# Kernel tuning notes

Hardware: AMD Instinct MI355X
Metric: run time of the kernel (lower is better)

Reference implementation:

```python
import jax, jax.numpy as jnp
import numpy as np

HIDDEN = 1024
HEADS = 16
DEPTH = HIDDEN // HEADS  # 64
B, S = 1, 2048  # batch must be 1: E is built with shape (heads, B*S, depth) and the skew reshape assumes B*S == S


def setup_inputs() -> dict:
    key = jax.random.key(0)
    ks = jax.random.split(key, 6)
    std = 0.02
    x = jax.random.normal(ks[0], (B, S, HIDDEN), dtype=jnp.float32)
    c_attn_w = jax.random.normal(ks[1], (HIDDEN, 3 * HIDDEN), dtype=jnp.float32) * std
    c_attn_b = jnp.zeros((1, 3 * HIDDEN), dtype=jnp.float32)
    c_proj_w = jax.random.normal(ks[2], (HIDDEN, HIDDEN), dtype=jnp.float32) * std
    c_proj_b = jnp.zeros((1, HIDDEN), dtype=jnp.float32)
    # GlorotUniform for E of shape (heads, B*S, depth)
    limit = float(np.sqrt(6.0 / (B * S + DEPTH)))
    E = jax.random.uniform(ks[3], (HEADS, B * S, DEPTH), dtype=jnp.float32,
                           minval=-limit, maxval=limit)
    return {"x": x, "c_attn_w": c_attn_w, "c_attn_b": c_attn_b,
            "c_proj_w": c_proj_w, "c_proj_b": c_proj_b, "E": E}


def _split_heads(t):
    # [B,S,H] -> [B,heads,S,depth]
    b, s, h = t.shape
    return t.reshape(b, s, HEADS, h // HEADS).transpose(0, 2, 1, 3)


def _relative_attention(q, E):
    # Transformer-XL style skewing. q: [B,heads,S,depth], E: [heads,B*S,depth]
    b, h, s, d = q.shape
    q_ = q.transpose(1, 0, 2, 3).reshape(h, b * s, d)
    rel = jnp.einsum('hnd,hmd->hnm', q_, E)            # [h, B*S, B*S]
    rel = rel.reshape(h, b, s, s)
    rel = jnp.pad(rel, ((0, 0), (0, 0), (0, 0), (1, 0)))  # pad left on last dim
    rel = rel.reshape(h, b, s + 1, s)[:, :, 1:]            # skew
    return rel.transpose(1, 0, 2, 3)                       # [B,heads,S,S]


def reference(x, c_attn_w, c_attn_b, c_proj_w, c_proj_b, E):
    b, s, hidden = x.shape
    qkv = x @ c_attn_w + c_attn_b                      # [B,S,3H]
    q, k, v = jnp.split(qkv, 3, axis=2)
    q, k, v = _split_heads(q), _split_heads(k), _split_heads(v)  # [B,h,S,d]

    w = jnp.einsum('bhqd,bhkd->bhqk', q, k)            # raw scores
    w = w + _relative_attention(q, E)
    w = w * jax.lax.rsqrt(jnp.asarray(DEPTH, w.dtype))  # scale applied after rel bias

    # causal mask: 1 in lower triangle (i >= j - ns + nd, nd == ns == S)
    i = jnp.arange(s)[:, None]
    j = jnp.arange(s)[None, :]
    bmask = (i >= j).astype(w.dtype)[None, None]        # [1,1,S,S]
    w = w * bmask - 10000.0 * (1.0 - bmask)

    a = jax.nn.softmax(w, axis=-1)                      # dropout is identity at inference
    ctx = jnp.einsum('bhqk,bhkd->bhqd', a, v)
    ctx = ctx.transpose(0, 2, 1, 3).reshape(b, s, hidden)  # merge heads
    out = ctx @ c_proj_w + c_proj_b
    return out
```

## Files before the change

### kernel.cpp

```cpp
#include <hip/hip_runtime.h>
#include <math.h>

#define SEQ  2048
#define NH   16
#define DEP  64
#define HID  1024

typedef __attribute__((ext_vector_type(8))) short s16x8;
typedef __attribute__((ext_vector_type(4))) float f32x4;

#define MFMA16(a, b, c) __builtin_amdgcn_mfma_f32_16x16x32_bf16(a, b, c, 0, 0, 0)
#define GLDS16(g, l)                                                           \
  __builtin_amdgcn_global_load_lds(                                            \
      (const __attribute__((address_space(1))) void*)(g),                      \
      (__attribute__((address_space(3))) void*)(l), 16, 0, 0)

__device__ __forceinline__ ushort f2b(float f) {
  union { float f; unsigned u; } x; x.f = f;
  unsigned r = (x.u + 0x7fff + ((x.u >> 16) & 1)) >> 16;
  return (ushort)r;
}
__device__ __forceinline__ float b2f(ushort u) {
  union { unsigned u; float f; } x; x.u = ((unsigned)u) << 16;
  return x.f;
}

__global__ __launch_bounds__(256) void prep(
    const float* __restrict__ x, ushort* __restrict__ xb,
    const float* __restrict__ E, ushort* __restrict__ Eb,
    const float* __restrict__ Wa, ushort* __restrict__ Wat,
    const float* __restrict__ Wp, ushort* __restrict__ Wpt) {
  const int bid = blockIdx.x, t = threadIdx.x;
  if (bid < 1024) {
    __shared__ float Ls[64 * 68];
    const float* in; ushort* out; int C, tile;
    if (bid < 768) { in = Wa; out = Wat; C = 3072; tile = bid; }
    else           { in = Wp; out = Wpt; C = 1024; tile = bid - 768; }
    const int ntx = C / 64;
    const int n0 = (tile % ntx) * 64, k0 = (tile / ntx) * 64;
    const int r = t >> 4, c4 = t & 15;
    #pragma unroll
    for (int p = 0; p < 4; p++) {
      float4 v = *(const float4*)&in[(size_t)(k0 + r + 16 * p) * C + n0 + c4 * 4];
      *(float4*)&Ls[(r + 16 * p) * 68 + c4 * 4] = v;
    }
    __syncthreads();
    #pragma unroll
    for (int p = 0; p < 4; p++) {
      int rw = r + 16 * p;
      ushort4 o;
      o.x = f2b(Ls[(c4 * 4 + 0) * 68 + rw]);
      o.y = f2b(Ls[(c4 * 4 + 1) * 68 + rw]);
      o.z = f2b(Ls[(c4 * 4 + 2) * 68 + rw]);
      o.w = f2b(Ls[(c4 * 4 + 3) * 68 + rw]);
      *(ushort4*)&out[(size_t)(n0 + rw) * 1024 + k0 + c4 * 4] = o;
    }
  } else {
    const int id = bid - 1024;
    #pragma unroll
    for (int rep = 0; rep < 4; rep++) {
      int i = id * 256 + t + rep * 262144;
      const float* src; ushort* dst; int k;
      if (i < 524288) { src = x; dst = xb; k = i; }
      else            { src = E; dst = Eb; k = i - 524288; }
      float4 v = *(const float4*)&src[(size_t)k * 4];
      ushort4 o = {f2b(v.x), f2b(v.y), f2b(v.z), f2b(v.w)};
      *(ushort4*)&dst[(size_t)k * 4] = o;
    }
  }
}

__global__ __launch_bounds__(256, 3) void gemm_qkv(
    const ushort* __restrict__ A, const ushort* __restrict__ Bt,
    const float* __restrict__ bias, int N, int K,
    ushort* __restrict__ qd, ushort* __restrict__ kd, ushort* __restrict__ vt) {
  __shared__ ushort As[2][64 * 64];
  __shared__ ushort Bs[2][128 * 64];
  const int t = threadIdx.x, l = t & 63, w = t >> 6;
  const int lr = l & 15, quad = l >> 4;
  const int row8 = l >> 3;
  const int chunk = (l & 7) ^ ((l >> 3) & 7);
  const int m0 = blockIdx.y * 64, n0 = blockIdx.x * 128;
  const int wr = (w >> 1) * 32, wc = (w & 1) * 64;
  f32x4 acc[2][4] = {};
  const ushort* gA = A + (size_t)m0 * K + chunk * 8;
  const ushort* gB = Bt + (size_t)n0 * K + chunk * 8;

  auto issue = [&](int buf, int k0) {
    #pragma unroll
    for (int g = 0; g < 2; g++) {
      int r = 16 * w + 8 * g + row8;
      GLDS16(gA + (size_t)r * K + k0, &As[buf][(16 * w + 8 * g) * 64]);
    }
    #pragma unroll
    for (int g = 0; g < 4; g++) {
      int r = 32 * w + 8 * g + row8;
      GLDS16(gB + (size_t)r * K + k0, &Bs[buf][(32 * w + 8 * g) * 64]);
    }
  };

  issue(0, 0);
  const int nsteps = K / 64;
  for (int s = 0; s < nsteps; s++) {
    __syncthreads();
    if (s + 1 < nsteps) issue((s + 1) & 1, (s + 1) * 64);
    const char* as_ = (const char*)As[s & 1];
    const char* bs_ = (const char*)Bs[s & 1];
    s16x8 af[2][2], bf[4][2];
    #pragma unroll
    for (int i = 0; i < 2; i++)
      #pragma unroll
      for (int hh = 0; hh < 2; hh++)
        af[i][hh] = *(const s16x8*)(as_ + (wr + 16 * i + lr) * 128 +
                                    (((4 * hh + quad) ^ (lr & 7)) * 16));
    #pragma unroll
    for (int j = 0; j < 4; j++)
      #pragma unroll
      for (int hh = 0; hh < 2; hh++)
        bf[j][hh] = *(const s16x8*)(bs_ + (wc + 16 * j + lr) * 128 +
                                    (((4 * hh + quad) ^ (lr & 7)) * 16));
    #pragma unroll
    for (int i = 0; i < 2; i++)
      #pragma unroll
      for (int j = 0; j < 4; j++) {
        acc[i][j] = MFMA16(af[i][0], bf[j][0], acc[i][j]);
        acc[i][j] = MFMA16(af[i][1], bf[j][1], acc[i][j]);
      }
  }

  #pragma unroll
  for (int i = 0; i < 2; i++) {
    #pragma unroll
    for (int j = 0; j < 4; j++) {
      const int colg = n0 + wc + 16 * j + lr;
      const float bb = bias[colg];
      const int rowg0 = m0 + wr + 16 * i + 4 * quad;
      const int part = colg >> 10, hh = (colg >> 6) & 15, d = colg & 63;
      if (part == 2) {
        ushort4 ov;
        ov.x = f2b(acc[i][j][0] + bb);
        ov.y = f2b(acc[i][j][1] + bb);
        ov.z = f2b(acc[i][j][2] + bb);
        ov.w = f2b(acc[i][j][3] + bb);
        *(ushort4*)&vt[((size_t)hh * 64 + d) * SEQ + rowg0] = ov;
      } else {
        ushort* dst = part == 0 ? qd : kd;
        const float sc = part == 0 ? 0.125f : 1.0f;
        #pragma unroll
        for (int r = 0; r < 4; r++)
          dst[((size_t)hh * SEQ + rowg0 + r) * 64 + d] = f2b((acc[i][j][r] + bb) * sc);
      }
    }
  }
}

__global__ __launch_bounds__(256, 3) void gemm_proj(
    const ushort* __restrict__ A, const ushort* __restrict__ Bt,
    const float* __restrict__ bias, float* __restrict__ Cout,
    const ushort* __restrict__ po, const float* __restrict__ pl) {
  const int K = HID, N = HID;
  __shared__ ushort As[2][64 * 64];
  __shared__ ushort Bs[2][64 * 64];
  const int t = threadIdx.x, l = t & 63, w = t >> 6;
  const int lr = l & 15, quad = l >> 4;
  const int row8 = l >> 3;
  const int chunk = (l & 7) ^ ((l >> 3) & 7);
  const int m0 = blockIdx.y * 64, n0 = blockIdx.x * 64;
  const int wr = (w >> 1) * 32, wc = (w & 1) * 32;
  f32x4 acc[2][2] = {};
  const bool mergeA = (m0 >= 1024);
  const int pp = 31 - (m0 >> 6);
  const int mr = t >> 2, mseg = t & 3;
  int4 ra0, ra1, rb0, rb1; float rinv;
  const ushort* gA = A + (size_t)m0 * K + chunk * 8;
  const ushort* gB = Bt + (size_t)n0 * K + chunk * 8;

  auto issueA = [&](int buf, int k0) {
    #pragma unroll
    for (int g = 0; g < 2; g++) {
      int r = 16 * w + 8 * g;
      GLDS16(gA + (size_t)(r + row8) * K + k0, &As[buf][r * 64]);
    }
  };
  auto issueB = [&](int buf, int k0) {
    #pragma unroll
    for (int g = 0; g < 2; g++) {
      int r = 16 * w + 8 * g;
      GLDS16(gB + (size_t)(r + row8) * K + k0, &Bs[buf][r * 64]);
    }
  };
  auto stageA_load = [&](int k0) {
    const int hd = k0 >> 6;
    const ushort* o0 = po + ((size_t)(hd * 16 + pp) * 2) * 4096 + mr * 64 + mseg * 16;
    ra0 = *(const int4*)o0;
    ra1 = *(const int4*)(o0 + 8);
    rb0 = *(const int4*)(o0 + 4096);
    rb1 = *(const int4*)(o0 + 4096 + 8);
    const float* plb = pl + ((size_t)(hd * 16 + pp) * 2) * 64;
    rinv = 1.0f / (plb[mr] + plb[64 + mr]);
  };
  auto stageA_write = [&](int buf) {
    ushort* dst = &As[buf][mr * 64];
    ushort ov[8];
    const ushort* sa = (const ushort*)&ra0;
    const ushort* sb = (const ushort*)&rb0;
    #pragma unroll
    for (int k = 0; k < 8; k++) ov[k] = f2b((b2f(sa[k]) + b2f(sb[k])) * rinv);
    *(int4*)&dst[((2 * mseg) ^ (mr & 7)) * 8] = *(const int4*)ov;
    sa = (const ushort*)&ra1;
    sb = (const ushort*)&rb1;
    #pragma unroll
    for (int k = 0; k < 8; k++) ov[k] = f2b((b2f(sa[k]) + b2f(sb[k])) * rinv);
    *(int4*)&dst[((2 * mseg + 1) ^ (mr & 7)) * 8] = *(const int4*)ov;
  };

  if (mergeA) stageA_load(0); else issueA(0, 0);
  issueB(0, 0);
  if (mergeA) stageA_write(0);
  const int nsteps = K / 64;
  for (int s = 0; s < nsteps; s++) {
    __syncthreads();
    const bool pref = (s + 1 < nsteps);
    if (pref) {
      if (mergeA) stageA_load((s + 1) * 64);
      else issueA((s + 1) & 1, (s + 1) * 64);
      issueB((s + 1) & 1, (s + 1) * 64);
    }
    const char* as_ = (const char*)As[s & 1];
    const char* bs_ = (const char*)Bs[s & 1];
    s16x8 af[2][2], bf[2][2];
    #pragma unroll
    for (int i = 0; i < 2; i++)
      #pragma unroll
      for (int hh = 0; hh < 2; hh++)
        af[i][hh] = *(const s16x8*)(as_ + (wr + 16 * i + lr) * 128 +
                                    (((4 * hh + quad) ^ (lr & 7)) * 16));
    #pragma unroll
    for (int j = 0; j < 2; j++)
      #pragma unroll
      for (int hh = 0; hh < 2; hh++)
        bf[j][hh] = *(const s16x8*)(bs_ + (wc + 16 * j + lr) * 128 +
                                    (((4 * hh + quad) ^ (lr & 7)) * 16));
    #pragma unroll
    for (int i = 0; i < 2; i++)
      #pragma unroll
      for (int j = 0; j < 2; j++) {
        acc[i][j] = MFMA16(af[i][0], bf[j][0], acc[i][j]);
        acc[i][j] = MFMA16(af[i][1], bf[j][1], acc[i][j]);
      }
    if (pref && mergeA) stageA_write((s + 1) & 1);
  }

  #pragma unroll
  for (int i = 0; i < 2; i++)
    #pragma unroll
    for (int j = 0; j < 2; j++) {
      const int colg = n0 + wc + 16 * j + lr;
      const float bb = bias[colg];
      const int rowg0 = m0 + wr + 16 * i + 4 * quad;
      #pragma unroll
      for (int r = 0; r < 4; r++)
        Cout[(size_t)(rowg0 + r) * N + colg] = acc[i][j][r] + bb;
    }
}

__global__ __launch_bounds__(256, 2) void attn_mfma(
    const ushort* __restrict__ qw, const ushort* __restrict__ kw,
    const ushort* __restrict__ vT, const ushort* __restrict__ Ebf,
    ushort* __restrict__ ctx, ushort* __restrict__ pa_o,
    float* __restrict__ pa_l) {
  __shared__ ushort KT[2][64 * 64];
  __shared__ ushort VS[2][64 * 64];
  __shared__ ushort EB[4][64 * 64];
  __shared__ ushort PB[4][16 * 72];
  const int t = threadIdx.x, l = t & 63, w = t >> 6;
  const int lr = l & 15, quad = l >> 4;
  const int row8 = l >> 3;
  const int chunk = (l & 7) ^ ((l >> 3) & 7);
  const int h = blockIdx.y;
  const int p = blockIdx.x >> 1, half = blockIdx.x & 1;
  const int i0A = 64 * p, i0B = 64 * (31 - p);

  int ph_i0[2], ph_k0[2], ph_k1[2], nph, tot;
  bool ph_diag[2], ph_dir[2];
  if (half == 0) {
    ph_i0[0] = i0A; ph_k0[0] = 0; ph_k1[0] = p + 1;  ph_diag[0] = true;  ph_dir[0] = true;
    ph_i0[1] = i0B; ph_k0[1] = 0; ph_k1[1] = 16 - p; ph_diag[1] = false; ph_dir[1] = false;
    nph = 2; tot = 17;
  } else {
    ph_i0[0] = i0B; ph_k0[0] = 16 - p; ph_k1[0] = 32 - p; ph_diag[0] = true; ph_dir[0] = false;
    ph_i0[1] = 0; ph_k0[1] = 0; ph_k1[1] = 0; ph_diag[1] = false; ph_dir[1] = false;
    nph = 1; tot = 16;
  }

  const ushort* kwh = kw + (size_t)h * SEQ * 64;
  const ushort* vgh = vT + (size_t)h * 64 * SEQ;
  const ushort* egh = Ebf + (size_t)h * SEQ * 64;

  auto issue_kv = [&](int buf, int j0) {
    const ushort* kb = kwh + (size_t)j0 * 64 + chunk * 8;
    const ushort* vb = vgh + j0 + chunk * 8;
    #pragma unroll
    for (int g = 0; g < 2; g++) {
      int r = 16 * w + 8 * g + row8;
      GLDS16(kb + (size_t)r * 64, &KT[buf][(16 * w + 8 * g) * 64]);
      GLDS16(vb + (size_t)r * SEQ, &VS[buf][(16 * w + 8 * g) * 64]);
    }
  };
  auto issue_e = [&](int slot, int r0) {
    #pragma unroll
    for (int g = 0; g < 2; g++) {
      int r = r0 + 16 * w + 8 * g + row8;
      if (r > SEQ - 1) r = SEQ - 1;
      GLDS16(egh + (size_t)r * 64 + chunk * 8, &EB[slot][(16 * w + 8 * g) * 64]);
    }
  };

  int pi = 0, kt = ph_k0[0], ebs = 0;
  {
    const int m0 = 1984 - ph_i0[0] + kt * 64;
    issue_kv(0, kt * 64);
    issue_e(0, m0);
    issue_e(1, m0 + 64);
  }

  s16x8 aq0, aq1;
  {
    const ushort* qg = qw + ((size_t)h * SEQ + ph_i0[0] + 16 * w) * 64;
    aq0 = *(const s16x8*)(qg + lr * 64 + quad * 8);
    aq1 = *(const s16x8*)(qg + lr * 64 + 32 + quad * 8);
  }

  f32x4 o[4] = {};
  float li[4] = {0.f, 0.f, 0.f, 0.f};
  f32x4 rtc = {};

  for (int s = 0; s < tot; s++) {
    __syncthreads();

    const int i0 = ph_i0[pi];
    const bool first = (kt == ph_k0[pi]);
    const bool last = (kt == ph_k1[pi] - 1);
    const bool diag = ph_diag[pi] && last;

    int ebs_next = ebs;
    {
      int npi = pi, nkt = kt + 1;
      bool have = true, newph = false;
      if (nkt == ph_k1[pi]) {
        if (pi + 1 < nph) { npi = pi + 1; nkt = ph_k0[npi]; newph = true; }
        else have = false;
      }
      if (have) {
        issue_kv((s + 1) & 1, nkt * 64);
        const int m0n = 1984 - ph_i0[npi] + nkt * 64;
        if (newph) {
          issue_e((ebs + 2) & 3, m0n);
          issue_e((ebs + 3) & 3, m0n + 64);
          ebs_next = (ebs + 2) & 3;
        } else {
          issue_e((ebs + 2) & 3, m0n + 64);
          ebs_next = (ebs + 1) & 3;
        }
      }
    }

    const char* KTc = (const char*)KT[s & 1];
    const char* VSc = (const char*)VS[s & 1];

    auto eb_frag = [&](int row, s16x8& e0, s16x8& e1) {
      const char* e_ = (const char*)EB[(ebs + (row >> 6)) & 3];
      const int rb = (row & 63) * 128;
      e0 = *(const s16x8*)(e_ + rb + ((quad ^ (lr & 7)) * 16));
      e1 = *(const s16x8*)(e_ + rb + (((4 + quad) ^ (lr & 7)) * 16));
    };

    f32x4 s4[4];
    #pragma unroll
    for (int b = 0; b < 4; b++) {
      const int row = 16 * b + lr;
      s16x8 bk0 = *(const s16x8*)(KTc + row * 128 + ((quad ^ (lr & 7)) * 16));
      s16x8 bk1 = *(const s16x8*)(KTc + row * 128 + (((4 + quad) ^ (lr & 7)) * 16));
      f32x4 z = {};
      z = MFMA16(aq0, bk0, z);
      z = MFMA16(aq1, bk1, z);
      s4[b] = z;
    }

    {
      const int ebase = 48 - 16 * w;
      f32x4 rt[5];
      if (first) {
        s16x8 e0, e1;
        eb_frag(ebase + lr, e0, e1);
        f32x4 z = {};
        z = MFMA16(aq0, e0, z);
        z = MFMA16(aq1, e1, z);
        rt[0] = z;
      } else {
        rt[0] = rtc;
      }
      #pragma unroll
      for (int b = 1; b < 5; b++) {
        s16x8 e0, e1;
        eb_frag(ebase + 16 * b + lr, e0, e1);
        f32x4 z = {};
        z = MFMA16(aq0, e0, z);
        z = MFMA16(aq1, e1, z);
        rt[b] = z;
      }
      rtc = rt[4];
      #pragma unroll
      for (int r = 0; r < 4; r++) {
        const int ti = 4 * quad + r;
        const int u = lr - ti + 15;
        const int src = (u & 15) | (l & 48);
        const float sh0 = __shfl(rt[0][r], src);
        const float sh1 = __shfl(rt[1][r], src);
        const float sh2 = __shfl(rt[2][r], src);
        const float sh3 = __shfl(rt[3][r], src);
        const float sh4 = __shfl(rt[4][r], src);
        s4[0][r] += (u < 16) ? sh0 : sh1;
        s4[1][r] += (u < 16) ? sh1 : sh2;
        s4[2][r] += (u < 16) ? sh2 : sh3;
        s4[3][r] += (u < 16) ? sh3 : sh4;
      }
    }

    if (diag) {
      #pragma unroll
      for (int b = 0; b < 4; b++)
        #pragma unroll
        for (int r = 0; r < 4; r++) {
          int ii = 16 * w + 4 * quad + r;
          if (16 * b + lr > ii) s4[b][r] = -10000.0f;
        }
    }

    #pragma unroll
    for (int b = 0; b < 4; b++)
      #pragma unroll
      for (int r = 0; r < 4; r++) {
        float pp = __expf(s4[b][r]);
        s4[b][r] = pp;
        li[r] += pp;
      }

    {
      char* Pw = (char*)PB[w];
      #pragma unroll
      for (int b = 0; b < 4; b++)
        #pragma unroll
        for (int r = 0; r < 4; r++)
          *(ushort*)(Pw + (4 * quad + r) * 144 + (16 * b + lr) * 2) = f2b(s4[b][r]);
      s16x8 pa0 = *(const s16x8*)(Pw + lr * 144 + quad * 16);
      s16x8 pa1 = *(const s16x8*)(Pw + lr * 144 + 64 + quad * 16);
      #pragma unroll
      for (int dc = 0; dc < 4; dc++) {
        const int row = 16 * dc + lr;
        s16x8 bv0 = *(const s16x8*)(VSc + row * 128 + ((quad ^ (lr & 7)) * 16));
        s16x8 bv1 = *(const s16x8*)(VSc + row * 128 + (((4 + quad) ^ (lr & 7)) * 16));
        o[dc] = MFMA16(pa0, bv0, o[dc]);
        o[dc] = MFMA16(pa1, bv1, o[dc]);
      }
    }

    if (last) {
      float lsum[4];
      #pragma unroll
      for (int r = 0; r < 4; r++) {
        float v = li[r];
        v += __shfl_xor(v, 1);
        v += __shfl_xor(v, 2);
        v += __shfl_xor(v, 4);
        v += __shfl_xor(v, 8);
        lsum[r] = v;
      }
      if (ph_dir[pi]) {
        #pragma unroll
        for (int r = 0; r < 4; r++) {
          float inv = 1.0f / lsum[r];
          #pragma unroll
          for (int dc = 0; dc < 4; dc++) {
            int row = i0 + 16 * w + 4 * quad + r;
            int col = h * 64 + 16 * dc + lr;
            ctx[(size_t)row * HID + col] = f2b(o[dc][r] * inv);
          }
        }
      } else {
        ushort* po = pa_o + (((size_t)(h * 16 + p) * 2 + half) * 4096);
        float* pl = pa_l + (((size_t)(h * 16 + p) * 2 + half) * 64);
        #pragma unroll
        for (int r = 0; r < 4; r++) {
          int row = 16 * w + 4 * quad + r;
          #pragma unroll
          for (int dc = 0; dc < 4; dc++)
            po[row * 64 + 16 * dc + lr] = f2b(o[dc][r]);
          if (lr == 0) pl[row] = lsum[r];
        }
      }
      #pragma unroll
      for (int dc = 0; dc < 4; dc++) o[dc] = (f32x4){0.f, 0.f, 0.f, 0.f};
      #pragma unroll
      for (int r = 0; r < 4; r++) li[r] = 0.f;
      if (pi + 1 < nph) {
        const ushort* qg = qw + ((size_t)h * SEQ + ph_i0[pi + 1] + 16 * w) * 64;
        aq0 = *(const s16x8*)(qg + lr * 64 + quad * 8);
        aq1 = *(const s16x8*)(qg + lr * 64 + 32 + quad * 8);
      }
    }

    if (kt + 1 == ph_k1[pi]) { pi++; kt = (pi < nph) ? ph_k0[pi] : 0; }
    else kt++;
    ebs = ebs_next;
  }
}

extern "C" void kernel_launch(void* const* d_in, const int* in_sizes, int n_in,
                              void* d_out, int out_size, void* d_ws, size_t ws_size,
                              hipStream_t stream) {
  (void)in_sizes; (void)n_in; (void)out_size; (void)ws_size;
  const float* x  = (const float*)d_in[0];
  const float* Wa = (const float*)d_in[1];
  const float* ba = (const float*)d_in[2];
  const float* Wp = (const float*)d_in[3];
  const float* bp = (const float*)d_in[4];
  const float* E  = (const float*)d_in[5];
  float* out = (float*)d_out;

  ushort* xb  = (ushort*)d_ws;
  ushort* ctx = xb;
  ushort* Wat = xb + (size_t)2 * 1024 * 1024;
  ushort* Wpt = Wat + (size_t)3 * 1024 * 1024;
  ushort* Ebf = Wpt + (size_t)1024 * 1024;
  ushort* qwp = Ebf + (size_t)2 * 1024 * 1024;
  ushort* kwp = qwp + (size_t)2 * 1024 * 1024;
  ushort* vTp = kwp + (size_t)2 * 1024 * 1024;
  ushort* pa_o = Wat;
  float*  pa_l = (float*)(Wat + (size_t)2 * 1024 * 1024);

  prep<<<2048, 256, 0, stream>>>(x, xb, E, Ebf, Wa, Wat, Wp, Wpt);
  gemm_qkv<<<dim3(24, 32), 256, 0, stream>>>(xb, Wat, ba, 3 * HID, HID,
                                             qwp, kwp, vTp);
  attn_mfma<<<dim3(32, NH), 256, 0, stream>>>(qwp, kwp, vTp, Ebf, ctx,
                                              pa_o, pa_l);
  gemm_proj<<<dim3(16, 32), 256, 0, stream>>>(ctx, Wpt, bp, out, pa_o, pa_l);
}
```

Before: 161.2 us.

## Split partial merge into own kernel, load V directly to registers, add setprio

Moves the merge of the two partial attention outputs out of the projection GEMM into a separate merge_p kernel, so gemm_proj becomes a plain double-buffered GLDS GEMM. In attention, V tiles are now read straight from global memory into registers instead of being staged through LDS, which cuts LDS traffic and footprint at the cost of uncoalesced global loads. It also raises wave priority around the MFMA sections with s_setprio. The extra launch and the register-held V loads may offset the savings.

Result: slower. 167.2 us (+3.7%).

```diff
diff --git a/kernel.cpp b/kernel.cpp
--- a/kernel.cpp
+++ b/kernel.cpp
@@ -156,8 +156,7 @@
 
 __global__ __launch_bounds__(256, 3) void gemm_proj(
     const ushort* __restrict__ A, const ushort* __restrict__ Bt,
-    const float* __restrict__ bias, float* __restrict__ Cout,
-    const ushort* __restrict__ po, const float* __restrict__ pl) {
+    const float* __restrict__ bias, float* __restrict__ Cout) {
   const int K = HID, N = HID;
   __shared__ ushort As[2][64 * 64];
   __shared__ ushort Bs[2][64 * 64];
@@ -168,64 +167,23 @@
   const int m0 = blockIdx.y * 64, n0 = blockIdx.x * 64;
   const int wr = (w >> 1) * 32, wc = (w & 1) * 32;
   f32x4 acc[2][2] = {};
-  const bool mergeA = (m0 >= 1024);
-  const int pp = 31 - (m0 >> 6);
-  const int mr = t >> 2, mseg = t & 3;
-  int4 ra0, ra1, rb0, rb1; float rinv;
   const ushort* gA = A + (size_t)m0 * K + chunk * 8;
   const ushort* gB = Bt + (size_t)n0 * K + chunk * 8;
 
-  auto issueA = [&](int buf, int k0) {
+  auto issue = [&](int buf, int k0) {
     #pragma unroll
     for (int g = 0; g < 2; g++) {
       int r = 16 * w + 8 * g;
       GLDS16(gA + (size_t)(r + row8) * K + k0, &As[buf][r * 64]);
+      GLDS16(gB + (size_t)(r + row8) * K + k0, &Bs[buf][r * 64]);
     }
   };
-  auto issueB = [&](int buf, int k0) {
-    #pragma unroll
-    for (int g = 0; g < 2; g++) {
-      int r = 16 * w + 8 * g;
-      GLDS16(gB + (size_t)(r + row8) * K + k0, &Bs[buf][r * 64]);
-    }
-  };
-  auto stageA_load = [&](int k0) {
-    const int hd = k0 >> 6;
-    const ushort* o0 = po + ((size_t)(hd * 16 + pp) * 2) * 4096 + mr * 64 + mseg * 16;
-    ra0 = *(const int4*)o0;
-    ra1 = *(const int4*)(o0 + 8);
-    rb0 = *(const int4*)(o0 + 4096);
-    rb1 = *(const int4*)(o0 + 4096 + 8);
-    const float* plb = pl + ((size_t)(hd * 16 + pp) * 2) * 64;
-    rinv = 1.0f / (plb[mr] + plb[64 + mr]);
-  };
-  auto stageA_write = [&](int buf) {
-    ushort* dst = &As[buf][mr * 64];
-    ushort ov[8];
-    const ushort* sa = (const ushort*)&ra0;
-    const ushort* sb = (const ushort*)&rb0;
-    #pragma unroll
-    for (int k = 0; k < 8; k++) ov[k] = f2b((b2f(sa[k]) + b2f(sb[k])) * rinv);
-    *(int4*)&dst[((2 * mseg) ^ (mr & 7)) * 8] = *(const int4*)ov;
-    sa = (const ushort*)&ra1;
-    sb = (const ushort*)&rb1;
-    #pragma unroll
-    for (int k = 0; k < 8; k++) ov[k] = f2b((b2f(sa[k]) + b2f(sb[k])) * rinv);
-    *(int4*)&dst[((2 * mseg + 1) ^ (mr & 7)) * 8] = *(const int4*)ov;
-  };
-
-  if (mergeA) stageA_load(0); else issueA(0, 0);
-  issueB(0, 0);
-  if (mergeA) stageA_write(0);
+
+  issue(0, 0);
   const int nsteps = K / 64;
   for (int s = 0; s < nsteps; s++) {
     __syncthreads();
-    const bool pref = (s + 1 < nsteps);
-    if (pref) {
-      if (mergeA) stageA_load((s + 1) * 64);
-      else issueA((s + 1) & 1, (s + 1) * 64);
-      issueB((s + 1) & 1, (s + 1) * 64);
-    }
+    if (s + 1 < nsteps) issue((s + 1) & 1, (s + 1) * 64);
     const char* as_ = (const char*)As[s & 1];
     const char* bs_ = (const char*)Bs[s & 1];
     s16x8 af[2][2], bf[2][2];
@@ -248,7 +206,6 @@
         acc[i][j] = MFMA16(af[i][0], bf[j][0], acc[i][j]);
         acc[i][j] = MFMA16(af[i][1], bf[j][1], acc[i][j]);
       }
-    if (pref && mergeA) stageA_write((s + 1) & 1);
   }
 
   #pragma unroll
@@ -270,7 +227,6 @@
     ushort* __restrict__ ctx, ushort* __restrict__ pa_o,
     float* __restrict__ pa_l) {
   __shared__ ushort KT[2][64 * 64];
-  __shared__ ushort VS[2][64 * 64];
   __shared__ ushort EB[4][64 * 64];
   __shared__ ushort PB[4][16 * 72];
   const int t = threadIdx.x, l = t & 63, w = t >> 6;
@@ -297,14 +253,12 @@
   const ushort* vgh = vT + (size_t)h * 64 * SEQ;
   const ushort* egh = Ebf + (size_t)h * SEQ * 64;
 
-  auto issue_kv = [&](int buf, int j0) {
+  auto issue_k = [&](int buf, int j0) {
     const ushort* kb = kwh + (size_t)j0 * 64 + chunk * 8;
-    const ushort* vb = vgh + j0 + chunk * 8;
     #pragma unroll
     for (int g = 0; g < 2; g++) {
       int r = 16 * w + 8 * g + row8;
       GLDS16(kb + (size_t)r * 64, &KT[buf][(16 * w + 8 * g) * 64]);
-      GLDS16(vb + (size_t)r * SEQ, &VS[buf][(16 * w + 8 * g) * 64]);
     }
   };
   auto issue_e = [&](int slot, int r0) {
@@ -319,7 +273,7 @@
   int pi = 0, kt = ph_k0[0], ebs = 0;
   {
     const int m0 = 1984 - ph_i0[0] + kt * 64;
-    issue_kv(0, kt * 64);
+    issue_k(0, kt * 64);
     issue_e(0, m0);
     issue_e(1, m0 + 64);
   }
@@ -342,6 +296,15 @@
     const bool first = (kt == ph_k0[pi]);
     const bool last = (kt == ph_k1[pi] - 1);
     const bool diag = ph_diag[pi] && last;
+    const int j0 = kt * 64;
+
+    s16x8 vv[4][2];
+    #pragma unroll
+    for (int dc = 0; dc < 4; dc++) {
+      const ushort* vr = vgh + (size_t)(16 * dc + lr) * SEQ + j0 + quad * 8;
+      vv[dc][0] = *(const s16x8*)vr;
+      vv[dc][1] = *(const s16x8*)(vr + 32);
+    }
 
     int ebs_next = ebs;
     {
@@ -352,7 +315,7 @@
         else have = false;
       }
       if (have) {
-        issue_kv((s + 1) & 1, nkt * 64);
+        issue_k((s + 1) & 1, nkt * 64);
         const int m0n = 1984 - ph_i0[npi] + nkt * 64;
         if (newph) {
           issue_e((ebs + 2) & 3, m0n);
@@ -366,7 +329,6 @@
     }
 
     const char* KTc = (const char*)KT[s & 1];
-    const char* VSc = (const char*)VS[s & 1];
 
     auto eb_frag = [&](int row, s16x8& e0, s16x8& e1) {
       const char* e_ = (const char*)EB[(ebs + (row >> 6)) & 3];
@@ -376,6 +338,7 @@
     };
 
     f32x4 s4[4];
+    __builtin_amdgcn_s_setprio(1);
     #pragma unroll
     for (int b = 0; b < 4; b++) {
       const int row = 16 * b + lr;
@@ -386,10 +349,12 @@
       z = MFMA16(aq1, bk1, z);
       s4[b] = z;
     }
+    __builtin_amdgcn_s_setprio(0);
 
     {
       const int ebase = 48 - 16 * w;
       f32x4 rt[5];
+      __builtin_amdgcn_s_setprio(1);
       if (first) {
         s16x8 e0, e1;
         eb_frag(ebase + lr, e0, e1);
@@ -409,6 +374,7 @@
         z = MFMA16(aq1, e1, z);
         rt[b] = z;
       }
+      __builtin_amdgcn_s_setprio(0);
       rtc = rt[4];
       #pragma unroll
       for (int r = 0; r < 4; r++) {
@@ -455,14 +421,13 @@
           *(ushort*)(Pw + (4 * quad + r) * 144 + (16 * b + lr) * 2) = f2b(s4[b][r]);
       s16x8 pa0 = *(const s16x8*)(Pw + lr * 144 + quad * 16);
       s16x8 pa1 = *(const s16x8*)(Pw + lr * 144 + 64 + quad * 16);
+      __builtin_amdgcn_s_setprio(1);
       #pragma unroll
       for (int dc = 0; dc < 4; dc++) {
-        const int row = 16 * dc + lr;
-        s16x8 bv0 = *(const s16x8*)(VSc + row * 128 + ((quad ^ (lr & 7)) * 16));
-        s16x8 bv1 = *(const s16x8*)(VSc + row * 128 + (((4 + quad) ^ (lr & 7)) * 16));
-        o[dc] = MFMA16(pa0, bv0, o[dc]);
-        o[dc] = MFMA16(pa1, bv1, o[dc]);
-      }
+        o[dc] = MFMA16(pa0, vv[dc][0], o[dc]);
+        o[dc] = MFMA16(pa1, vv[dc][1], o[dc]);
+      }
+      __builtin_amdgcn_s_setprio(0);
     }
 
     if (last) {
@@ -516,6 +481,28 @@
   }
 }
 
+__global__ __launch_bounds__(256) void merge_p(const ushort* __restrict__ pa_o,
+                                               const float* __restrict__ pa_l,
+                                               ushort* __restrict__ ctx) {
+  const int p = blockIdx.x, h = blockIdx.y, t = threadIdx.x;
+  const int row = t >> 2, seg = t & 3;
+  const ushort* o0 = pa_o + ((size_t)(h * 16 + p) * 2 + 0) * 4096;
+  const ushort* o1 = pa_o + ((size_t)(h * 16 + p) * 2 + 1) * 4096;
+  const float* l0 = pa_l + ((size_t)(h * 16 + p) * 2 + 0) * 64;
+  const float* l1 = pa_l + ((size_t)(h * 16 + p) * 2 + 1) * 64;
+  const float inv = 1.0f / (l0[row] + l1[row]);
+  const int i0b = 64 * (31 - p);
+  #pragma unroll
+  for (int g = 0; g < 2; g++) {
+    ushort a[8], b[8], r[8];
+    *(int4*)a = *(const int4*)&o0[row * 64 + seg * 16 + g * 8];
+    *(int4*)b = *(const int4*)&o1[row * 64 + seg * 16 + g * 8];
+    #pragma unroll
+    for (int j = 0; j < 8; j++) r[j] = f2b((b2f(a[j]) + b2f(b[j])) * inv);
+    *(int4*)&ctx[(size_t)(i0b + row) * HID + h * 64 + seg * 16 + g * 8] = *(int4*)r;
+  }
+}
+
 extern "C" void kernel_launch(void* const* d_in, const int* in_sizes, int n_in,
                               void* d_out, int out_size, void* d_ws, size_t ws_size,
                               hipStream_t stream) {
@@ -544,5 +531,6 @@
                                              qwp, kwp, vTp);
   attn_mfma<<<dim3(32, NH), 256, 0, stream>>>(qwp, kwp, vTp, Ebf, ctx,
                                               pa_o, pa_l);
-  gemm_proj<<<dim3(16, 32), 256, 0, stream>>>(ctx, Wpt, bp, out, pa_o, pa_l);
-}
+  merge_p<<<dim3(16, NH), 256, 0, stream>>>(pa_o, pa_l, ctx);
+  gemm_proj<<<dim3(16, 32), 256, 0, stream>>>(ctx, Wpt, bp, out);
+}
```
